# Optimization experiments

Hardware: AMD Instinct MI355X
Metric: run time of the kernel (lower is better)

## Reference

```python
import jax, jax.numpy as jnp
import numpy as np

KERNEL_LEN = 128
INPUT_LEN = 1_000_000
MAX_PATH = 30          # hardcoded self.max_path in the module
PATH_NUM = 10          # self.path_num / out_len
L = INPUT_LEN + KERNEL_LEN  # max possible DTW path length


def setup_inputs() -> dict:
    key = jax.random.key(0)
    k1, k2, k3, k4, k5 = jax.random.split(key, 5)
    kernel = jax.random.normal(k1, (KERNEL_LEN,), dtype=jnp.float32)
    x = jax.random.normal(k2, (INPUT_LEN,), dtype=jnp.float32)
    # path indices produced by the external DP library (opaque int outputs)
    path_k = jax.random.randint(k3, (MAX_PATH, L), 0, KERNEL_LEN, dtype=jnp.int32)
    path_i = jax.random.randint(k4, (MAX_PATH, L), 0, INPUT_LEN, dtype=jnp.int32)
    path_length = jax.random.randint(k5, (MAX_PATH,), 0, L, dtype=jnp.int32)
    return {"kernel": kernel, "x": x, "path_k": path_k, "path_i": path_i,
            "path_length": path_length, "path_num": 12}


def reference(kernel, x, path_k, path_i, path_length, path_num):
    # out[k] = sum_{i < path_length[k]} (kernel[path_k[k,i]] - x[path_i[k,i]])**2
    # for k < min(path_num, PATH_NUM); remaining entries stay zero.
    n = min(int(path_num), PATH_NUM)
    pk = path_k[:PATH_NUM]                      # [PATH_NUM, L]
    pi = path_i[:PATH_NUM]
    step_mask = jnp.arange(L)[None, :] < path_length[:PATH_NUM, None]  # ragged lengths
    diff = kernel[pk] - x[pi]                   # gather + elementwise, [PATH_NUM, L]
    sq = jnp.where(step_mask, diff * diff, jnp.float32(0))
    out = sq.sum(axis=1)                        # [PATH_NUM]
    k_mask = jnp.arange(PATH_NUM) < n
    return jnp.where(k_mask, out, jnp.float32(0))
```

## Files before the change

kernel.cpp:

```cpp
#include <hip/hip_runtime.h>

#define KERNEL_LEN 128
#define INPUT_LEN 1000000
#define PATH_NUM 10
#define L_TOTAL (INPUT_LEN + KERNEL_LEN)
#define BLOCKS_PER_PATH 128
#define BLOCK_SIZE 256

__global__ __launch_bounds__(BLOCK_SIZE) void dtw_spring_npath_kernel(
    const float* __restrict__ kern,
    const float* __restrict__ x,
    const int*   __restrict__ path_k,
    const int*   __restrict__ path_i,
    const int*   __restrict__ path_length,
    const int*   __restrict__ path_num,
    float*       __restrict__ out)
{
    __shared__ float k_lds[KERNEL_LEN];
    const int tid = threadIdx.x;
    if (tid < KERNEL_LEN) k_lds[tid] = kern[tid];
    __syncthreads();

    const int p = blockIdx.y;
    const int n = min(path_num[0], PATH_NUM);
    if (p >= n) return;

    const int len  = path_length[p];
    const int len4 = len & ~3;

    const int* __restrict__ pk = path_k + (size_t)p * L_TOTAL;
    const int* __restrict__ pi = path_i + (size_t)p * L_TOTAL;

    float acc = 0.0f;
    const int stride = gridDim.x * BLOCK_SIZE * 4;
    for (int t = (blockIdx.x * BLOCK_SIZE + tid) * 4; t < len4; t += stride) {
        const int4 vk = *reinterpret_cast<const int4*>(pk + t);
        const int4 vi = *reinterpret_cast<const int4*>(pi + t);
        float d0 = k_lds[vk.x] - x[vi.x];
        float d1 = k_lds[vk.y] - x[vi.y];
        float d2 = k_lds[vk.z] - x[vi.z];
        float d3 = k_lds[vk.w] - x[vi.w];
        acc += d0 * d0 + d1 * d1 + d2 * d2 + d3 * d3;
    }
    if (blockIdx.x == 0 && tid < (len - len4)) {
        const int t = len4 + tid;
        const float d = k_lds[pk[t]] - x[pi[t]];
        acc += d * d;
    }

    #pragma unroll
    for (int off = 32; off > 0; off >>= 1)
        acc += __shfl_down(acc, off, 64);

    __shared__ float wsum[BLOCK_SIZE / 64];
    const int wave = tid >> 6;
    if ((tid & 63) == 0) wsum[wave] = acc;
    __syncthreads();
    if (tid == 0) {
        float s = 0.0f;
        #pragma unroll
        for (int w = 0; w < BLOCK_SIZE / 64; ++w) s += wsum[w];
        atomicAdd(&out[p], s);
    }
}

extern "C" void kernel_launch(void* const* d_in, const int* in_sizes, int n_in,
                              void* d_out, int out_size, void* d_ws, size_t ws_size,
                              hipStream_t stream) {
    const float* kern        = (const float*)d_in[0];
    const float* x           = (const float*)d_in[1];
    const int*   path_k      = (const int*)d_in[2];
    const int*   path_i      = (const int*)d_in[3];
    const int*   path_length = (const int*)d_in[4];
    const int*   path_num    = (const int*)d_in[5];
    float*       out         = (float*)d_out;

    hipMemsetAsync(out, 0, (size_t)out_size * sizeof(float), stream);

    dim3 grid(BLOCKS_PER_PATH, PATH_NUM);
    dim3 block(BLOCK_SIZE);
    dtw_spring_npath_kernel<<<grid, block, 0, stream>>>(
        kern, x, path_k, path_i, path_length, path_num, out);
}
```

Measured before the change: 50.41 us.

## Flatten grid so each block processes all paths over a shared index range

```diff
diff --git a/kernel.cpp b/kernel.cpp
--- a/kernel.cpp
+++ b/kernel.cpp
@@ -4,8 +4,11 @@
 #define INPUT_LEN 1000000
 #define PATH_NUM 10
 #define L_TOTAL (INPUT_LEN + KERNEL_LEN)
-#define BLOCKS_PER_PATH 128
+#define NBLOCKS 2048
 #define BLOCK_SIZE 256
+#define CHUNK 4
+
+typedef int v4i __attribute__((ext_vector_type(4)));
 
 __global__ __launch_bounds__(BLOCK_SIZE) void dtw_spring_npath_kernel(
     const float* __restrict__ kern,
@@ -21,46 +24,66 @@
     if (tid < KERNEL_LEN) k_lds[tid] = kern[tid];
     __syncthreads();
 
-    const int p = blockIdx.y;
     const int n = min(path_num[0], PATH_NUM);
-    if (p >= n) return;
 
-    const int len  = path_length[p];
-    const int len4 = len & ~3;
+    float acc[PATH_NUM];
+    #pragma unroll
+    for (int p = 0; p < PATH_NUM; ++p) acc[p] = 0.0f;
 
-    const int* __restrict__ pk = path_k + (size_t)p * L_TOTAL;
-    const int* __restrict__ pi = path_i + (size_t)p * L_TOTAL;
+    const int start  = (blockIdx.x * BLOCK_SIZE + tid) * CHUNK;
+    const int stride = NBLOCKS * BLOCK_SIZE * CHUNK;
 
-    float acc = 0.0f;
-    const int stride = gridDim.x * BLOCK_SIZE * 4;
-    for (int t = (blockIdx.x * BLOCK_SIZE + tid) * 4; t < len4; t += stride) {
-        const int4 vk = *reinterpret_cast<const int4*>(pk + t);
-        const int4 vi = *reinterpret_cast<const int4*>(pi + t);
-        float d0 = k_lds[vk.x] - x[vi.x];
-        float d1 = k_lds[vk.y] - x[vi.y];
-        float d2 = k_lds[vk.z] - x[vi.z];
-        float d3 = k_lds[vk.w] - x[vi.w];
-        acc += d0 * d0 + d1 * d1 + d2 * d2 + d3 * d3;
-    }
-    if (blockIdx.x == 0 && tid < (len - len4)) {
-        const int t = len4 + tid;
-        const float d = k_lds[pk[t]] - x[pi[t]];
-        acc += d * d;
+    #pragma unroll
+    for (int p = 0; p < PATH_NUM; ++p) {
+        if (p < n) {
+            const int len  = path_length[p];
+            const int len4 = len & ~(CHUNK - 1);
+            const int* __restrict__ pk = path_k + (size_t)p * L_TOTAL;
+            const int* __restrict__ pi = path_i + (size_t)p * L_TOTAL;
+
+            float a = 0.0f;
+            for (int t = start; t < len4; t += stride) {
+                const v4i ik = *reinterpret_cast<const v4i*>(pk + t);
+                const v4i ii = *reinterpret_cast<const v4i*>(pi + t);
+                const float x0 = x[(unsigned)ii[0]];
+                const float x1 = x[(unsigned)ii[1]];
+                const float x2 = x[(unsigned)ii[2]];
+                const float x3 = x[(unsigned)ii[3]];
+                const float d0 = k_lds[(unsigned)ik[0]] - x0;
+                const float d1 = k_lds[(unsigned)ik[1]] - x1;
+                const float d2 = k_lds[(unsigned)ik[2]] - x2;
+                const float d3 = k_lds[(unsigned)ik[3]] - x3;
+                a = fmaf(d0, d0, a);
+                a = fmaf(d1, d1, a);
+                a = fmaf(d2, d2, a);
+                a = fmaf(d3, d3, a);
+            }
+            if (blockIdx.x == 0) {
+                const int t = len4 + tid;
+                if (t < len) {
+                    const float d = k_lds[pk[t]] - x[pi[t]];
+                    a = fmaf(d, d, a);
+                }
+            }
+            acc[p] = a;
+        }
     }
 
+    __shared__ float wsum[PATH_NUM][BLOCK_SIZE / 64];
+    const int wave = tid >> 6;
+    const int lane = tid & 63;
     #pragma unroll
-    for (int off = 32; off > 0; off >>= 1)
-        acc += __shfl_down(acc, off, 64);
-
-    __shared__ float wsum[BLOCK_SIZE / 64];
-    const int wave = tid >> 6;
-    if ((tid & 63) == 0) wsum[wave] = acc;
+    for (int p = 0; p < PATH_NUM; ++p) {
+        float a = acc[p];
+        #pragma unroll
+        for (int off = 32; off > 0; off >>= 1)
+            a += __shfl_down(a, off, 64);
+        if (lane == 0) wsum[p][wave] = a;
+    }
     __syncthreads();
-    if (tid == 0) {
-        float s = 0.0f;
-        #pragma unroll
-        for (int w = 0; w < BLOCK_SIZE / 64; ++w) s += wsum[w];
-        atomicAdd(&out[p], s);
+    if (tid < PATH_NUM && tid < n) {
+        const float s = wsum[tid][0] + wsum[tid][1] + wsum[tid][2] + wsum[tid][3];
+        if (s != 0.0f) atomicAdd(&out[tid], s);
     }
 }
 
@@ -77,8 +100,6 @@
 
     hipMemsetAsync(out, 0, (size_t)out_size * sizeof(float), stream);
 
-    dim3 grid(BLOCKS_PER_PATH, PATH_NUM);
-    dim3 block(BLOCK_SIZE);
-    dtw_spring_npath_kernel<<<grid, block, 0, stream>>>(
+    dtw_spring_npath_kernel<<<dim3(NBLOCKS), dim3(BLOCK_SIZE), 0, stream>>>(
         kern, x, path_k, path_i, path_length, path_num, out);
 }
```

Result: slower. 53.83 us (+6.8%).
